# Kernel optimization log

Measured on AMD Instinct MI355X. Metric: run time of the kernel, lower is better.

Reference implementation:

```python
import jax, jax.numpy as jnp
import numpy as np

NX, NY, NZ = 512, 512, 1
C_BEV = 128
C_BEFORE = C_BEV // NZ  # features per z-slice
B = 4
P_PER_BATCH = 80000


def setup_inputs() -> dict:
    key = jax.random.key(0)
    P = B * P_PER_BATCH
    pillar_features = jax.random.normal(key, (P, C_BEFORE), dtype=jnp.float32)
    # Build coords with unique spatial cells per batch so scatter order is irrelevant.
    rng = np.random.default_rng(0)
    cells = NZ * NY * NX
    coords_np = np.empty((P, 4), dtype=np.int32)
    for b in range(B):  # loop over tiny fixed batch count, setup only
        flat = rng.choice(cells, size=P_PER_BATCH, replace=False)
        z = flat // (NY * NX)
        y = (flat // NX) % NY
        x = flat % NX
        s = slice(b * P_PER_BATCH, (b + 1) * P_PER_BATCH)
        coords_np[s, 0] = b
        coords_np[s, 1] = z
        coords_np[s, 2] = y
        coords_np[s, 3] = x
    return {
        "batch_size": B,
        "pillar_features": pillar_features,
        "coords": jnp.asarray(coords_np),
    }


def reference(batch_size, pillar_features, coords):
    # Fused single-pass scatter: global flat index = b*(nz*ny*nx) + z*ny*nx + y*nx + x
    cells = NZ * NY * NX
    flat = (coords[:, 0].astype(jnp.int32) * cells
            + coords[:, 1].astype(jnp.int32) * (NY * NX)
            + coords[:, 2].astype(jnp.int32) * NX
            + coords[:, 3].astype(jnp.int32))
    canvas = jnp.zeros((batch_size * cells, C_BEFORE), dtype=pillar_features.dtype)
    canvas = canvas.at[flat].set(pillar_features)
    # [B*nz*ny*nx, C] -> [B, nz, ny, nx, C] -> [B, C, nz, ny, nx] -> [B, C*nz, ny, nx]
    canvas = canvas.reshape(batch_size, NZ, NY, NX, C_BEFORE)
    canvas = jnp.transpose(canvas, (0, 4, 1, 2, 3))
    return canvas.reshape(batch_size, C_BEFORE * NZ, NY, NX)
```

## Files before the change

### kernel.cpp

```cpp
#include <hip/hip_runtime.h>


#define NXD 512
#define NYD 512
#define NZD 1
#define CB  128
#define CELLS (NXD * NYD * NZD)

__global__ void k_scatter_idx(const int* __restrict__ coords,
                              int* __restrict__ map, int P) {
    int p = blockIdx.x * blockDim.x + threadIdx.x;
    if (p >= P) return;
    int4 c = ((const int4*)coords)[p];
    int cell = c.y * (NYD * NXD) + c.z * NXD + c.w;
    map[c.x * CELLS + cell] = p;
}

__global__ __launch_bounds__(256) void k_gather(const float* __restrict__ feat,
                                                const int* __restrict__ map,
                                                float* __restrict__ out) {
    __shared__ int    pidx[64];
    __shared__ float4 tile4[64 * 32];

    const int t = threadIdx.x;
    const int tiles_per_b = CELLS / 64;
    const int b = blockIdx.x / tiles_per_b;
    const int cell_base = (blockIdx.x % tiles_per_b) * 64;

    if (t < 64) pidx[t] = map[b * CELLS + cell_base + t];
    __syncthreads();

    {
        const int c4 = t & 31;
        const int r0 = t >> 5;
        #pragma unroll
        for (int rr = 0; rr < 8; ++rr) {
            const int x = rr * 8 + r0;
            const int idx = pidx[x];
            float4 v = make_float4(0.f, 0.f, 0.f, 0.f);
            if (idx >= 0) v = ((const float4*)feat)[(size_t)idx * (CB / 4) + c4];
            tile4[x * 32 + (c4 ^ (x >> 2))] = v;
        }
    }
    __syncthreads();

    {
        const int x4 = t & 15;
        const int cr = t >> 4;
        float* outb = out + (size_t)b * (size_t)CB * CELLS + cell_base + x4 * 4;
        #pragma unroll
        for (int cc = 0; cc < 8; ++cc) {
            const int c  = cc * 16 + cr;
            const int c4 = c >> 2;
            const int ce = c & 3;
            float4 v;
            v.x = ((const float*)&tile4[(x4 * 4 + 0) * 32 + (c4 ^ x4)])[ce];
            v.y = ((const float*)&tile4[(x4 * 4 + 1) * 32 + (c4 ^ x4)])[ce];
            v.z = ((const float*)&tile4[(x4 * 4 + 2) * 32 + (c4 ^ x4)])[ce];
            v.w = ((const float*)&tile4[(x4 * 4 + 3) * 32 + (c4 ^ x4)])[ce];
            *reinterpret_cast<float4*>(outb + (size_t)c * CELLS) = v;
        }
    }
}

extern "C" void kernel_launch(void* const* d_in, const int* in_sizes, int n_in,
                              void* d_out, int out_size, void* d_ws, size_t ws_size,
                              hipStream_t stream) {
    const float* feat   = (const float*)d_in[1];
    const int*   coords = (const int*)d_in[2];
    float*       out    = (float*)d_out;
    int*         map    = (int*)d_ws;

    const int B = out_size / (CB * CELLS);
    const int P = in_sizes[1] / CB;
    const int n_map = B * CELLS;

    hipMemsetAsync(map, 0xFF, (size_t)n_map * sizeof(int), stream);
    k_scatter_idx<<<(P + 255) / 256, 256, 0, stream>>>(coords, map, P);
    k_gather<<<B * (CELLS / 64), 256, 0, stream>>>(feat, map, out);
}
```

Baseline: 185.8 us.

## Widen gather tile to 256 cells and transpose through LDS in channel slices

```diff
diff --git a/kernel.cpp b/kernel.cpp
--- a/kernel.cpp
+++ b/kernel.cpp
@@ -6,6 +6,11 @@
 #define NZD 1
 #define CB  128
 #define CELLS (NXD * NYD * NZD)
+
+#define TILE  256
+#define SLICE 32
+#define PADF  4
+#define ROWF  (TILE + PADF)
 
 __global__ void k_scatter_idx(const int* __restrict__ coords,
                               int* __restrict__ map, int P) {
@@ -19,47 +24,51 @@
 __global__ __launch_bounds__(256) void k_gather(const float* __restrict__ feat,
                                                 const int* __restrict__ map,
                                                 float* __restrict__ out) {
-    __shared__ int    pidx[64];
-    __shared__ float4 tile4[64 * 32];
+    __shared__ int   pidx[TILE];
+    __shared__ float ldsT[SLICE * ROWF];
 
     const int t = threadIdx.x;
-    const int tiles_per_b = CELLS / 64;
+    const int tiles_per_b = CELLS / TILE;
     const int b = blockIdx.x / tiles_per_b;
-    const int cell_base = (blockIdx.x % tiles_per_b) * 64;
+    const int cell_base = (blockIdx.x % tiles_per_b) * TILE;
 
-    if (t < 64) pidx[t] = map[b * CELLS + cell_base + t];
+    pidx[t] = map[b * CELLS + cell_base + t];
     __syncthreads();
 
-    {
-        const int c4 = t & 31;
-        const int r0 = t >> 5;
+    const int c4    = t & 7;
+    const int cell0 = t >> 3;
+    const int x4    = t & 63;
+    const int chr   = t >> 6;
+
+    int idxr[8];
+    #pragma unroll
+    for (int rr = 0; rr < 8; ++rr) idxr[rr] = pidx[rr * 32 + cell0];
+
+    float* outb = out + (size_t)b * CB * CELLS + cell_base;
+
+    #pragma unroll
+    for (int ci = 0; ci < 4; ++ci) {
         #pragma unroll
         for (int rr = 0; rr < 8; ++rr) {
-            const int x = rr * 8 + r0;
-            const int idx = pidx[x];
+            const int cell = rr * 32 + cell0;
+            const int idx  = idxr[rr];
             float4 v = make_float4(0.f, 0.f, 0.f, 0.f);
-            if (idx >= 0) v = ((const float4*)feat)[(size_t)idx * (CB / 4) + c4];
-            tile4[x * 32 + (c4 ^ (x >> 2))] = v;
+            if (idx >= 0)
+                v = ((const float4*)feat)[(size_t)idx * (CB / 4) + ci * 8 + c4];
+            ldsT[(c4 * 4 + 0) * ROWF + cell] = v.x;
+            ldsT[(c4 * 4 + 1) * ROWF + cell] = v.y;
+            ldsT[(c4 * 4 + 2) * ROWF + cell] = v.z;
+            ldsT[(c4 * 4 + 3) * ROWF + cell] = v.w;
         }
-    }
-    __syncthreads();
+        __syncthreads();
 
-    {
-        const int x4 = t & 15;
-        const int cr = t >> 4;
-        float* outb = out + (size_t)b * (size_t)CB * CELLS + cell_base + x4 * 4;
         #pragma unroll
         for (int cc = 0; cc < 8; ++cc) {
-            const int c  = cc * 16 + cr;
-            const int c4 = c >> 2;
-            const int ce = c & 3;
-            float4 v;
-            v.x = ((const float*)&tile4[(x4 * 4 + 0) * 32 + (c4 ^ x4)])[ce];
-            v.y = ((const float*)&tile4[(x4 * 4 + 1) * 32 + (c4 ^ x4)])[ce];
-            v.z = ((const float*)&tile4[(x4 * 4 + 2) * 32 + (c4 ^ x4)])[ce];
-            v.w = ((const float*)&tile4[(x4 * 4 + 3) * 32 + (c4 ^ x4)])[ce];
-            *reinterpret_cast<float4*>(outb + (size_t)c * CELLS) = v;
+            const int c = cc * 4 + chr;
+            float4 v = *(const float4*)&ldsT[c * ROWF + x4 * 4];
+            *reinterpret_cast<float4*>(outb + (size_t)(ci * SLICE + c) * CELLS + x4 * 4) = v;
         }
+        __syncthreads();
     }
 }
 
@@ -77,5 +86,5 @@
 
     hipMemsetAsync(map, 0xFF, (size_t)n_map * sizeof(int), stream);
     k_scatter_idx<<<(P + 255) / 256, 256, 0, stream>>>(coords, map, P);
-    k_gather<<<B * (CELLS / 64), 256, 0, stream>>>(feat, map, out);
+    k_gather<<<B * (CELLS / TILE), 256, 0, stream>>>(feat, map, out);
 }
```

New measurement: 209.1 us. +12.5%, slower.
